# Kernel tuning notes

Hardware: AMD Instinct MI355X
Metric: run time of the kernel (lower is better)

The kernel has to match this reference:

```python
import jax, jax.numpy as jnp
import numpy as np

N = 500_000          # minibatch nodes
NUM_NODES = 1_000_000  # embedding table rows
F0 = 500_000         # raw feature table rows for ntype 0
DIN = 256            # raw feature dim for ntype 0
D = 128              # embed_size


def setup_inputs() -> dict:
    key = jax.random.key(0)
    k0, k1, k2, k3, k4, k5 = jax.random.split(key, 6)
    feat0 = jax.random.normal(k0, (F0, DIN), dtype=jnp.float32)
    # xavier-uniform-ish scale for the projection
    lim = float(np.sqrt(6.0 / (DIN + D)))
    W0 = jax.random.uniform(k1, (DIN, D), dtype=jnp.float32, minval=-lim, maxval=lim)
    # node_embeds initialized uniform(-1, 1)
    emb_table = jax.random.uniform(k2, (NUM_NODES, D), dtype=jnp.float32, minval=-1.0, maxval=1.0)
    node_ids = jax.random.randint(k3, (N,), 0, NUM_NODES, dtype=jnp.int32)
    node_tids = jax.random.randint(k4, (N,), 0, 2, dtype=jnp.int32)
    type_ids = jax.random.randint(k5, (N,), 0, F0, dtype=jnp.int32)
    return {"feat0": feat0, "W0": W0, "emb_table": emb_table,
            "node_ids": node_ids, "node_tids": node_tids, "type_ids": type_ids}


def reference(feat0, W0, emb_table, node_ids, node_tids, type_ids):
    # Original loops over node types, building per-type blocks and an index
    # map idx so that the final embeds[idx] restores the original node order.
    # That is equivalent to, per node i:
    #   out[i] = feat0[type_ids[i]] @ W0   if node_tids[i] == 0 (featured type)
    #   out[i] = emb_table[node_ids[i]]    if node_tids[i] == 1 (featureless)
    proj = feat0[type_ids] @ W0          # [N, D] gather + tall-skinny matmul
    emb = emb_table[node_ids]            # [N, D] embedding lookup
    is_featured = (node_tids == 0)[:, None]
    return jnp.where(is_featured, proj, emb)
```

## Files before the change

kernel.cpp:

```cpp
#include <hip/hip_runtime.h>
#include <hip/hip_bf16.h>

#define DIN 256
#define DOUT 128

using short8  = __attribute__((ext_vector_type(8))) short;
using floatx4 = __attribute__((ext_vector_type(4))) float;

__device__ __forceinline__ unsigned short f2bf(float f) {
    union { float f; unsigned u; } x; x.f = f;
    unsigned u = x.u;
    unsigned r = u + 0x7fffu + ((u >> 16) & 1u);
    return (unsigned short)(r >> 16);
}

__device__ __forceinline__ unsigned cvt2(float x, float y) {
    union { __hip_bfloat162 h2; unsigned u; } c;
    c.h2 = __float22bfloat162_rn(float2{x, y});
    return c.u;
}

__global__ void w0_pack_kernel(const float* __restrict__ W0,
                               unsigned short* __restrict__ Bfrag) {
    int e = blockIdx.x * blockDim.x + threadIdx.x;
    int j  = e & 7;
    int l  = (e >> 3) & 63;
    int ks = (e >> 9) & 7;
    int ct = e >> 12;
    int k = ks * 32 + (l >> 4) * 8 + j;
    int c = ct * 16 + (l & 15);
    Bfrag[e] = f2bf(W0[k * DOUT + c]);
}

__global__ __launch_bounds__(512, 4) void fused_embed_kernel(
    const float* __restrict__ feat0,
    const float* __restrict__ emb_table,
    const unsigned short* __restrict__ Bfrag,
    const int* __restrict__ node_ids,
    const int* __restrict__ node_tids,
    const int* __restrict__ type_ids,
    float* __restrict__ out,
    int n)
{
    __shared__ short8 sB[4096];

    const int t  = threadIdx.x;
    const int w  = t >> 6;
    const int l  = t & 63;
    const int lr = l & 15;
    const int kg = l >> 4;

    const long long nodebase = (long long)blockIdx.x * 128 + w * 16;
    const long long myrow = nodebase + lr;
    int tid = 1, gt = 0, gn = 0;
    if (myrow < n) {
        tid = node_tids[myrow];
        gt  = type_ids[myrow];
        gn  = node_ids[myrow];
    }

    {
        const short8* src = reinterpret_cast<const short8*>(Bfrag);
        short8 tmp[8];
        #pragma unroll
        for (int j = 0; j < 8; ++j) tmp[j] = src[t + j * 512];
        #pragma unroll
        for (int j = 0; j < 8; ++j) sB[t + j * 512] = tmp[j];
    }

    __syncthreads();

    const int gts = (tid == 0) ? gt : 0;
    const float4* arow = reinterpret_cast<const float4*>(
        feat0 + (long long)gts * DIN) + kg * 2;
    float4 av[16];
    #pragma unroll
    for (int ks = 0; ks < 8; ++ks) {
        av[2 * ks]     = arow[ks * 8];
        av[2 * ks + 1] = arow[ks * 8 + 1];
    }

    const int crow = l >> 2;
    const int csub = l & 3;
    const int t_c  = __shfl(tid, crow);
    const int gn_c = __shfl(gn, crow);
    const long long cnode = nodebase + crow;
    const bool copyrow = (t_c == 1) && (cnode < n);
    const int  gns = copyrow ? gn_c : 0;
    const float4* esrc = reinterpret_cast<const float4*>(
        emb_table + (long long)gns * DOUT);
    float4 ev[8];
    #pragma unroll
    for (int j = 0; j < 8; ++j) ev[j] = esrc[csub + j * 4];

    floatx4 acc[8];
    #pragma unroll
    for (int ct = 0; ct < 8; ++ct) acc[ct] = (floatx4){0.f, 0.f, 0.f, 0.f};
    #pragma unroll
    for (int ks = 0; ks < 8; ++ks) {
        const float4 a0 = av[2 * ks];
        const float4 a1 = av[2 * ks + 1];
        union { short8 s; unsigned u[4]; } af;
        af.u[0] = cvt2(a0.x, a0.y);
        af.u[1] = cvt2(a0.z, a0.w);
        af.u[2] = cvt2(a1.x, a1.y);
        af.u[3] = cvt2(a1.z, a1.w);
        #pragma unroll
        for (int ct = 0; ct < 8; ++ct)
            acc[ct] = __builtin_amdgcn_mfma_f32_16x16x32_bf16(
                af.s, sB[(ct * 8 + ks) * 64 + l], acc[ct], 0, 0, 0);
    }

    #pragma unroll
    for (int r = 0; r < 4; ++r) {
        const int row = kg * 4 + r;
        const int t_r = __shfl(tid, row);
        const long long node = nodebase + row;
        if (t_r == 0 && node < n) {
            float* orow = out + node * DOUT;
            #pragma unroll
            for (int ct = 0; ct < 8; ++ct)
                orow[ct * 16 + lr] = acc[ct][r];
        }
    }

    if (copyrow) {
        float4* dst = reinterpret_cast<float4*>(out + cnode * DOUT);
        #pragma unroll
        for (int j = 0; j < 8; ++j) dst[csub + j * 4] = ev[j];
    }
}

extern "C" void kernel_launch(void* const* d_in, const int* in_sizes, int n_in,
                              void* d_out, int out_size, void* d_ws, size_t ws_size,
                              hipStream_t stream) {
    const float* feat0      = (const float*)d_in[0];
    const float* W0         = (const float*)d_in[1];
    const float* emb_table  = (const float*)d_in[2];
    const int*   node_ids   = (const int*)d_in[3];
    const int*   node_tids  = (const int*)d_in[4];
    const int*   type_ids   = (const int*)d_in[5];
    float*       out        = (float*)d_out;
    const int n = in_sizes[3];

    unsigned short* Bfrag = (unsigned short*)d_ws;

    hipLaunchKernelGGL(w0_pack_kernel, dim3((DIN * DOUT) / 256), dim3(256),
                       0, stream, W0, Bfrag);

    const int grid = (n + 127) / 128;
    hipLaunchKernelGGL(fused_embed_kernel, dim3(grid), dim3(512), 0, stream,
                       feat0, emb_table, Bfrag, node_ids, node_tids, type_ids,
                       out, n);
}
```

Before: 156.3 us.

## Process multiple 16-row tiles per wave to amortize W0 LDS staging

Each wave now loops over T=4 consecutive 16-node tiles instead of one, so each block handles 512 nodes and the 64KB W0 fragment copy into shared memory is amortized over four times more work. The next tile's node index/type loads are prefetched during the current tile's MFMA compute. The grid shrinks by four, which reduces parallelism and the latency hiding that comes from many resident blocks, while the per-tile gathers remain serialized inside the loop.

```diff
diff --git a/kernel.cpp b/kernel.cpp
--- a/kernel.cpp
+++ b/kernel.cpp
@@ -40,23 +40,23 @@
     const int* __restrict__ node_tids,
     const int* __restrict__ type_ids,
     float* __restrict__ out,
-    int n)
+    int n, int T)
 {
     __shared__ short8 sB[4096];
 
-    const int t  = threadIdx.x;
-    const int w  = t >> 6;
-    const int l  = t & 63;
-    const int lr = l & 15;
-    const int kg = l >> 4;
+    const int t    = threadIdx.x;
+    const int w    = t >> 6;
+    const int l    = t & 63;
+    const int lr   = l & 15;
+    const int kg   = l >> 4;
+    const int crow = l >> 2;
+    const int csub = l & 3;
 
-    const long long nodebase = (long long)blockIdx.x * 128 + w * 16;
-    const long long myrow = nodebase + lr;
-    int tid = 1, gt = 0, gn = 0;
-    if (myrow < n) {
-        tid = node_tids[myrow];
-        gt  = type_ids[myrow];
-        gn  = node_ids[myrow];
+    const long long wbase = ((long long)blockIdx.x * 8 + w) * ((long long)T * 16);
+    int tid = -1, gt = 0, gn = 0;
+    {
+        const long long row0 = wbase + lr;
+        if (row0 < n) { tid = node_tids[row0]; gt = type_ids[row0]; gn = node_ids[row0]; }
     }
 
     {
@@ -70,64 +70,74 @@
 
     __syncthreads();
 
-    const int gts = (tid == 0) ? gt : 0;
-    const float4* arow = reinterpret_cast<const float4*>(
-        feat0 + (long long)gts * DIN) + kg * 2;
-    float4 av[16];
-    #pragma unroll
-    for (int ks = 0; ks < 8; ++ks) {
-        av[2 * ks]     = arow[ks * 8];
-        av[2 * ks + 1] = arow[ks * 8 + 1];
-    }
+    for (int tt = 0; tt < T; ++tt) {
+        const long long nodebase = wbase + (long long)tt * 16;
 
-    const int crow = l >> 2;
-    const int csub = l & 3;
-    const int t_c  = __shfl(tid, crow);
-    const int gn_c = __shfl(gn, crow);
-    const long long cnode = nodebase + crow;
-    const bool copyrow = (t_c == 1) && (cnode < n);
-    const int  gns = copyrow ? gn_c : 0;
-    const float4* esrc = reinterpret_cast<const float4*>(
-        emb_table + (long long)gns * DOUT);
-    float4 ev[8];
-    #pragma unroll
-    for (int j = 0; j < 8; ++j) ev[j] = esrc[csub + j * 4];
+        const int gts = (tid == 0) ? gt : 0;
+        const float4* arow = reinterpret_cast<const float4*>(
+            feat0 + (long long)gts * DIN) + kg * 2;
+        float4 av[16];
+        #pragma unroll
+        for (int ks = 0; ks < 8; ++ks) {
+            av[2 * ks]     = arow[ks * 8];
+            av[2 * ks + 1] = arow[ks * 8 + 1];
+        }
 
-    floatx4 acc[8];
-    #pragma unroll
-    for (int ct = 0; ct < 8; ++ct) acc[ct] = (floatx4){0.f, 0.f, 0.f, 0.f};
-    #pragma unroll
-    for (int ks = 0; ks < 8; ++ks) {
-        const float4 a0 = av[2 * ks];
-        const float4 a1 = av[2 * ks + 1];
-        union { short8 s; unsigned u[4]; } af;
-        af.u[0] = cvt2(a0.x, a0.y);
-        af.u[1] = cvt2(a0.z, a0.w);
-        af.u[2] = cvt2(a1.x, a1.y);
-        af.u[3] = cvt2(a1.z, a1.w);
+        const int t_c  = __shfl(tid, crow);
+        const int gn_c = __shfl(gn, crow);
+        const long long cnode = nodebase + crow;
+        const bool copyrow = (t_c == 1) && (cnode < n);
+        const int  gns = copyrow ? gn_c : 0;
+        const float4* esrc = reinterpret_cast<const float4*>(
+            emb_table + (long long)gns * DOUT);
+        float4 ev[8];
         #pragma unroll
-        for (int ct = 0; ct < 8; ++ct)
-            acc[ct] = __builtin_amdgcn_mfma_f32_16x16x32_bf16(
-                af.s, sB[(ct * 8 + ks) * 64 + l], acc[ct], 0, 0, 0);
-    }
+        for (int j = 0; j < 8; ++j) ev[j] = esrc[csub + j * 4];
 
-    #pragma unroll
-    for (int r = 0; r < 4; ++r) {
-        const int row = kg * 4 + r;
-        const int t_r = __shfl(tid, row);
-        const long long node = nodebase + row;
-        if (t_r == 0 && node < n) {
-            float* orow = out + node * DOUT;
+        const int tidS = tid;
+
+        if (tt + 1 < T) {
+            const long long rown = nodebase + 16 + lr;
+            tid = -1;
+            if (rown < n) { tid = node_tids[rown]; gt = type_ids[rown]; gn = node_ids[rown]; }
+        }
+
+        floatx4 acc[8];
+        #pragma unroll
+        for (int ct = 0; ct < 8; ++ct) acc[ct] = (floatx4){0.f, 0.f, 0.f, 0.f};
+        #pragma unroll
+        for (int ks = 0; ks < 8; ++ks) {
+            const float4 a0 = av[2 * ks];
+            const float4 a1 = av[2 * ks + 1];
+            union { short8 s; unsigned u[4]; } af;
+            af.u[0] = cvt2(a0.x, a0.y);
+            af.u[1] = cvt2(a0.z, a0.w);
+            af.u[2] = cvt2(a1.x, a1.y);
+            af.u[3] = cvt2(a1.z, a1.w);
             #pragma unroll
             for (int ct = 0; ct < 8; ++ct)
-                orow[ct * 16 + lr] = acc[ct][r];
+                acc[ct] = __builtin_amdgcn_mfma_f32_16x16x32_bf16(
+                    af.s, sB[(ct * 8 + ks) * 64 + l], acc[ct], 0, 0, 0);
         }
-    }
 
-    if (copyrow) {
-        float4* dst = reinterpret_cast<float4*>(out + cnode * DOUT);
         #pragma unroll
-        for (int j = 0; j < 8; ++j) dst[csub + j * 4] = ev[j];
+        for (int r = 0; r < 4; ++r) {
+            const int row = kg * 4 + r;
+            const int t_r = __shfl(tidS, row);
+            const long long node = nodebase + row;
+            if (t_r == 0 && node < n) {
+                float* orow = out + node * DOUT;
+                #pragma unroll
+                for (int ct = 0; ct < 8; ++ct)
+                    orow[ct * 16 + lr] = acc[ct][r];
+            }
+        }
+
+        if (copyrow) {
+            float4* dst = reinterpret_cast<float4*>(out + cnode * DOUT);
+            #pragma unroll
+            for (int j = 0; j < 8; ++j) dst[csub + j * 4] = ev[j];
+        }
     }
 }
 
@@ -148,8 +158,10 @@
     hipLaunchKernelGGL(w0_pack_kernel, dim3((DIN * DOUT) / 256), dim3(256),
                        0, stream, W0, Bfrag);
 
-    const int grid = (n + 127) / 128;
+    const int T = 4;
+    const int wtiles = (n + 15) / 16;
+    const int grid = (wtiles + 8 * T - 1) / (8 * T);
     hipLaunchKernelGGL(fused_embed_kernel, dim3(grid), dim3(512), 0, stream,
                        feat0, emb_table, Bfrag, node_ids, node_tids, type_ids,
-                       out, n);
+                       out, n, T);
 }
```

Result: slower. 604.7 us (+286.8%).

## Persistent tiles with double-buffered LDS gather of feature rows

Applied to the files above, without the earlier changes.

Restructures the fused kernel so each block walks 16 tiles of 32 nodes. Each wave keeps its own slice of the W0 bf16 fragments in registers for all tiles instead of staging the full matrix in LDS per block. Feature rows are gathered straight into double-buffered, XOR-swizzled LDS with global_load_lds, and the next tile's gather and indices are prefetched while the current tile runs its MFMAs. The aim is to amortize weight loading and hide gather latency, at the cost of a barrier per tile, 64KB of LDS per block and fewer, longer-lived blocks.

```diff
diff --git a/kernel.cpp b/kernel.cpp
--- a/kernel.cpp
+++ b/kernel.cpp
@@ -3,6 +3,8 @@
 
 #define DIN 256
 #define DOUT 128
+#define ROWS 32
+#define TPB  16
 
 using short8  = __attribute__((ext_vector_type(8))) short;
 using floatx4 = __attribute__((ext_vector_type(4))) float;
@@ -40,9 +42,9 @@
     const int* __restrict__ node_tids,
     const int* __restrict__ type_ids,
     float* __restrict__ out,
-    int n)
+    int n, long long ntiles)
 {
-    __shared__ short8 sB[4096];
+    __shared__ float sA[2][ROWS * DIN];
 
     const int t  = threadIdx.x;
     const int w  = t >> 6;
@@ -50,84 +52,111 @@
     const int lr = l & 15;
     const int kg = l >> 4;
 
-    const long long nodebase = (long long)blockIdx.x * 128 + w * 16;
-    const long long myrow = nodebase + lr;
-    int tid = 1, gt = 0, gn = 0;
-    if (myrow < n) {
-        tid = node_tids[myrow];
-        gt  = type_ids[myrow];
-        gn  = node_ids[myrow];
+    short8 bf[8];
+    {
+        const short8* bsrc = reinterpret_cast<const short8*>(Bfrag);
+        #pragma unroll
+        for (int ks = 0; ks < 8; ++ks)
+            bf[ks] = bsrc[(w * 8 + ks) * 64 + l];
     }
 
-    {
-        const short8* src = reinterpret_cast<const short8*>(Bfrag);
-        short8 tmp[8];
+    const long long tile0   = (long long)blockIdx.x * TPB;
+    const long long tileEnd = (tile0 + TPB < ntiles) ? tile0 + TPB : ntiles;
+    if (tile0 >= tileEnd) return;
+
+    auto loadIdx = [&](long long tt, int& tid, int& gt, int& gn) {
+        tid = -1; gt = 0; gn = 0;
+        const long long node = tt * ROWS + (l & 31);
+        if (node < n) { tid = node_tids[node]; gt = type_ids[node]; gn = node_ids[node]; }
+    };
+
+    auto issueDMA = [&](int buf, int tidN, int gtN) {
         #pragma unroll
-        for (int j = 0; j < 8; ++j) tmp[j] = src[t + j * 512];
-        #pragma unroll
-        for (int j = 0; j < 8; ++j) sB[t + j * 512] = tmp[j];
-    }
+        for (int rj = 0; rj < 4; ++rj) {
+            const int row  = w * 4 + rj;
+            const int tidr = __shfl(tidN, row);
+            const int gtr  = __shfl(gtN, row);
+            const int gts  = (tidr == 0) ? gtr : 0;
+            const float* gsrc = feat0 + (long long)gts * DIN
+                                + ((l ^ (row & 7)) << 2);
+            __builtin_amdgcn_global_load_lds(
+                (const __attribute__((address_space(1))) unsigned int*)gsrc,
+                (__attribute__((address_space(3))) unsigned int*)(&sA[buf][row * DIN]),
+                16, 0, 0);
+        }
+    };
 
+    int tidC, gtC, gnC, tidN, gtN, gnN;
+    loadIdx(tile0, tidC, gtC, gnC);
+    if (tile0 + 1 < tileEnd) loadIdx(tile0 + 1, tidN, gtN, gnN);
+    else { tidN = -1; gtN = 0; gnN = 0; }
+    issueDMA(0, tidC, gtC);
     __syncthreads();
 
-    const int gts = (tid == 0) ? gt : 0;
-    const float4* arow = reinterpret_cast<const float4*>(
-        feat0 + (long long)gts * DIN) + kg * 2;
-    float4 av[16];
-    #pragma unroll
-    for (int ks = 0; ks < 8; ++ks) {
-        av[2 * ks]     = arow[ks * 8];
-        av[2 * ks + 1] = arow[ks * 8 + 1];
-    }
+    for (long long tt = tile0; tt < tileEnd; ++tt) {
+        const int cur = (int)((tt - tile0) & 1);
 
-    const int crow = l >> 2;
-    const int csub = l & 3;
-    const int t_c  = __shfl(tid, crow);
-    const int gn_c = __shfl(gn, crow);
-    const long long cnode = nodebase + crow;
-    const bool copyrow = (t_c == 1) && (cnode < n);
-    const int  gns = copyrow ? gn_c : 0;
-    const float4* esrc = reinterpret_cast<const float4*>(
-        emb_table + (long long)gns * DOUT);
-    float4 ev[8];
-    #pragma unroll
-    for (int j = 0; j < 8; ++j) ev[j] = esrc[csub + j * 4];
+        if (tt + 1 < tileEnd) issueDMA(cur ^ 1, tidN, gtN);
 
-    floatx4 acc[8];
-    #pragma unroll
-    for (int ct = 0; ct < 8; ++ct) acc[ct] = (floatx4){0.f, 0.f, 0.f, 0.f};
-    #pragma unroll
-    for (int ks = 0; ks < 8; ++ks) {
-        const float4 a0 = av[2 * ks];
-        const float4 a1 = av[2 * ks + 1];
-        union { short8 s; unsigned u[4]; } af;
-        af.u[0] = cvt2(a0.x, a0.y);
-        af.u[1] = cvt2(a0.z, a0.w);
-        af.u[2] = cvt2(a1.x, a1.y);
-        af.u[3] = cvt2(a1.z, a1.w);
+        const int crow = w * 4 + (l >> 4);
+        const int csub = l & 15;
+        const int t_c  = __shfl(tidC, crow);
+        const int gn_c = __shfl(gnC, crow);
+        const long long cnode = tt * ROWS + crow;
+        const bool copyrow = (t_c == 1) && (cnode < n);
+        const float4* esrc = reinterpret_cast<const float4*>(
+            emb_table + (long long)(copyrow ? gn_c : 0) * DOUT) + csub * 2;
+        const float4 e0 = esrc[0];
+        const float4 e1 = esrc[1];
+
+        int tid2, gt2, gn2;
+        if (tt + 2 < tileEnd) loadIdx(tt + 2, tid2, gt2, gn2);
+        else { tid2 = -1; gt2 = 0; gn2 = 0; }
+
+        floatx4 acc[2];
+        acc[0] = (floatx4){0.f, 0.f, 0.f, 0.f};
+        acc[1] = (floatx4){0.f, 0.f, 0.f, 0.f};
+        const char* abase = reinterpret_cast<const char*>(&sA[cur][0]);
         #pragma unroll
-        for (int ct = 0; ct < 8; ++ct)
-            acc[ct] = __builtin_amdgcn_mfma_f32_16x16x32_bf16(
-                af.s, sB[(ct * 8 + ks) * 64 + l], acc[ct], 0, 0, 0);
-    }
+        for (int ks = 0; ks < 8; ++ks) {
+            #pragma unroll
+            for (int rt = 0; rt < 2; ++rt) {
+                const int row = rt * 16 + lr;
+                const int c0  = ks * 8 + kg * 2;
+                const unsigned a0 = (unsigned)(row * 1024) + (unsigned)(((c0)     ^ (row & 7)) << 4);
+                const unsigned a1 = (unsigned)(row * 1024) + (unsigned)(((c0 + 1) ^ (row & 7)) << 4);
+                const float4 f0 = *reinterpret_cast<const float4*>(abase + a0);
+                const float4 f1 = *reinterpret_cast<const float4*>(abase + a1);
+                union { short8 s; unsigned u[4]; } af;
+                af.u[0] = cvt2(f0.x, f0.y);
+                af.u[1] = cvt2(f0.z, f0.w);
+                af.u[2] = cvt2(f1.x, f1.y);
+                af.u[3] = cvt2(f1.z, f1.w);
+                acc[rt] = __builtin_amdgcn_mfma_f32_16x16x32_bf16(
+                    af.s, bf[ks], acc[rt], 0, 0, 0);
+            }
+        }
 
-    #pragma unroll
-    for (int r = 0; r < 4; ++r) {
-        const int row = kg * 4 + r;
-        const int t_r = __shfl(tid, row);
-        const long long node = nodebase + row;
-        if (t_r == 0 && node < n) {
-            float* orow = out + node * DOUT;
+        #pragma unroll
+        for (int rt = 0; rt < 2; ++rt) {
             #pragma unroll
-            for (int ct = 0; ct < 8; ++ct)
-                orow[ct * 16 + lr] = acc[ct][r];
+            for (int r = 0; r < 4; ++r) {
+                const int row = rt * 16 + kg * 4 + r;
+                const int t_r = __shfl(tidC, row);
+                const long long node = tt * ROWS + row;
+                if (t_r == 0 && node < n)
+                    out[node * DOUT + w * 16 + lr] = acc[rt][r];
+            }
         }
-    }
 
-    if (copyrow) {
-        float4* dst = reinterpret_cast<float4*>(out + cnode * DOUT);
-        #pragma unroll
-        for (int j = 0; j < 8; ++j) dst[csub + j * 4] = ev[j];
+        if (copyrow) {
+            float4* dst = reinterpret_cast<float4*>(out + cnode * DOUT) + csub * 2;
+            dst[0] = e0; dst[1] = e1;
+        }
+
+        tidC = tidN; gtC = gtN; gnC = gnN;
+        tidN = tid2; gtN = gt2; gnN = gn2;
+        __syncthreads();
     }
 }
 
@@ -148,8 +177,9 @@
     hipLaunchKernelGGL(w0_pack_kernel, dim3((DIN * DOUT) / 256), dim3(256),
                        0, stream, W0, Bfrag);
 
-    const int grid = (n + 127) / 128;
+    const long long ntiles = (n + ROWS - 1) / ROWS;
+    const int grid = (int)((ntiles + TPB - 1) / TPB);
     hipLaunchKernelGGL(fused_embed_kernel, dim3(grid), dim3(512), 0, stream,
                        feat0, emb_table, Bfrag, node_ids, node_tids, type_ids,
-                       out, n);
+                       out, n, ntiles);
 }
```

After: 159.7 us. 2.2% more time.
